# Kernel optimization log

Measured on AMD Instinct MI355X. Metric: run time of the kernel, lower is better.

The kernel has to match this reference:

```python
import jax, jax.numpy as jnp
import numpy as np

EMBED = 1024
HEADS = 16
HDIM = EMBED // HEADS
WIN = 14
RANK = 16
ALPHA = 32
MLP = 4 * EMBED


def setup_inputs() -> dict:
    key = jax.random.key(0)
    ks = jax.random.split(key, 10)
    s = 0.02
    return {
        "x": jax.random.normal(ks[0], (2, 64, 64, EMBED), jnp.float32),
        "norm1_g": jnp.ones((EMBED,), jnp.float32),
        "norm1_b": jnp.zeros((EMBED,), jnp.float32),
        "qkv_w": jax.random.normal(ks[1], (EMBED, 3 * EMBED), jnp.float32) * s,
        "qkv_b": jnp.zeros((3 * EMBED,), jnp.float32),
        "lora_a": jax.random.normal(ks[2], (EMBED, RANK), jnp.float32) * s,
        "lora_b": jax.random.normal(ks[3], (RANK, 3 * EMBED), jnp.float32) * s,
        "rel_pos_h": jax.random.normal(ks[4], (2 * WIN - 1, HDIM), jnp.float32) * s,
        "rel_pos_w": jax.random.normal(ks[5], (2 * WIN - 1, HDIM), jnp.float32) * s,
        "proj_w": jax.random.normal(ks[6], (EMBED, EMBED), jnp.float32) * s,
        "proj_b": jnp.zeros((EMBED,), jnp.float32),
        "norm2_g": jnp.ones((EMBED,), jnp.float32),
        "norm2_b": jnp.zeros((EMBED,), jnp.float32),
        "mlp_w1": jax.random.normal(ks[7], (EMBED, MLP), jnp.float32) * s,
        "mlp_b1": jnp.zeros((MLP,), jnp.float32),
        "mlp_w2": jax.random.normal(ks[8], (MLP, EMBED), jnp.float32) * s,
        "mlp_b2": jnp.zeros((EMBED,), jnp.float32),
    }


def layer_norm(x, g, b, eps=1e-6):
    mu = jnp.mean(x, axis=-1, keepdims=True)
    var = jnp.var(x, axis=-1, keepdims=True)
    return (x - mu) * jax.lax.rsqrt(var + eps) * g + b


def window_partition(x, w):
    B, H, W, C = x.shape
    ph, pw = (w - H % w) % w, (w - W % w) % w
    x = jnp.pad(x, ((0, 0), (0, ph), (0, pw), (0, 0)))
    Hp, Wp = H + ph, W + pw
    x = x.reshape(B, Hp // w, w, Wp // w, w, C)
    x = x.transpose(0, 1, 3, 2, 4, 5).reshape(-1, w, w, C)
    return x, (Hp, Wp)


def window_unpartition(x, w, pad_hw, hw):
    Hp, Wp = pad_hw
    H, W = hw
    B = x.shape[0] // (Hp // w * (Wp // w))
    x = x.reshape(B, Hp // w, Wp // w, w, w, -1)
    x = x.transpose(0, 1, 3, 2, 4, 5).reshape(B, Hp, Wp, -1)
    return x[:, :H, :W, :]


def _rel_table(rel_pos, size):
    # square windows, no interpolation: table is (2*size-1, dim)
    idx = jnp.arange(size)[:, None] - jnp.arange(size)[None, :] + (size - 1)
    return rel_pos[idx]  # (size, size, dim)


def reference(x, norm1_g, norm1_b, qkv_w, qkv_b, lora_a, lora_b,
              rel_pos_h, rel_pos_w, proj_w, proj_b, norm2_g, norm2_b,
              mlp_w1, mlp_b1, mlp_w2, mlp_b2):
    shortcut = x
    xn = layer_norm(x, norm1_g, norm1_b)
    h, w = xn.shape[1], xn.shape[2]
    xw, pad_hw = window_partition(xn, WIN)
    Bw, H, W, C = xw.shape
    N = H * W
    xf = xw.reshape(Bw, N, C)
    # QKV with LoRA injection: qkv(x) + (x @ A @ B) * alpha/rank
    qkv = xf @ qkv_w + qkv_b + (xf @ lora_a @ lora_b) * (ALPHA / RANK)
    qkv = qkv.reshape(Bw, N, 3, HEADS, HDIM).transpose(2, 0, 3, 1, 4)  # 3,Bw,h,N,d
    q, k, v = qkv[0], qkv[1], qkv[2]
    scale = HDIM ** -0.5
    attn = jnp.einsum('bhnd,bhmd->bhnm', q * scale, k)  # (Bw,heads,N,N)
    # decomposed relative position bias
    Rh = _rel_table(rel_pos_h, H)  # (H,H,d)
    Rw = _rel_table(rel_pos_w, W)  # (W,W,d)
    rq = q.reshape(Bw, HEADS, H, W, HDIM)
    rel_h = jnp.einsum('bhxyd,xkd->bhxyk', rq, Rh)  # (Bw,heads,H,W,H)
    rel_w = jnp.einsum('bhxyd,ykd->bhxyk', rq, Rw)  # (Bw,heads,H,W,W)
    attn = (attn.reshape(Bw, HEADS, H, W, H, W)
            + rel_h[..., :, None] + rel_w[..., None, :]).reshape(Bw, HEADS, N, N)
    attn = jax.nn.softmax(attn, axis=-1)
    out = jnp.einsum('bhnm,bhmd->bhnd', attn, v)
    out = out.reshape(Bw, HEADS, H, W, HDIM).transpose(0, 2, 3, 1, 4).reshape(Bw, H, W, C)
    out = out @ proj_w + proj_b
    out = window_unpartition(out, WIN, pad_hw, (h, w))
    x = shortcut + out
    # MLP with exact GELU (torch default)
    xn2 = layer_norm(x, norm2_g, norm2_b)
    hmid = jax.nn.gelu(xn2 @ mlp_w1 + mlp_b1, approximate=False)
    x = x + (hmid @ mlp_w2 + mlp_b2)
    return x
```

## Files before the change

### kernel.cpp

```cpp
#include <hip/hip_runtime.h>
#include <cstdint>
#include <cstddef>


typedef __bf16 bf16x8 __attribute__((ext_vector_type(8)));
typedef float f32x4 __attribute__((ext_vector_type(4)));

__device__ __forceinline__ unsigned short f2bf(float f) {
    unsigned u = __float_as_uint(f);
    u = (u + 0x7fffu + ((u >> 16) & 1u)) >> 16;
    return (unsigned short)u;
}
__device__ __forceinline__ float bf2f(unsigned short h) {
    return __uint_as_float(((unsigned)h) << 16);
}

#define GLDS16(gp, lp) __builtin_amdgcn_global_load_lds( \
    (__attribute__((address_space(1))) unsigned int*)(gp), \
    (__attribute__((address_space(3))) unsigned int*)(lp), 16, 0, 0)

__global__ __launch_bounds__(256) void weff_kernel(
    const float* __restrict__ W, const float* __restrict__ la,
    const float* __restrict__ lb, unsigned short* __restrict__ Wt)
{
    __shared__ float tile[32][33];
    __shared__ float lat[32][16];
    __shared__ float lbt[16][32];
    const int kb = blockIdx.x * 32, nb = blockIdx.y * 32;
    const int tn = threadIdx.x & 31, tk = threadIdx.x >> 5;
    for (int i = threadIdx.x; i < 32 * 16; i += 256)
        lat[i >> 4][i & 15] = la[(size_t)(kb + (i >> 4)) * 16 + (i & 15)];
    for (int i = threadIdx.x; i < 16 * 32; i += 256)
        lbt[i >> 5][i & 31] = lb[(size_t)(i >> 5) * 3072 + nb + (i & 31)];
#pragma unroll
    for (int i = 0; i < 4; ++i) {
        int k = tk + i * 8;
        tile[k][tn] = W[(size_t)(kb + k) * 3072 + nb + tn];
    }
    __syncthreads();
#pragma unroll
    for (int i = 0; i < 4; ++i) {
        int n = tk + i * 8;
        float acc = tile[tn][n];
#pragma unroll
        for (int r = 0; r < 16; ++r) acc += 2.0f * lat[tn][r] * lbt[r][n];
        Wt[(size_t)(nb + n) * 1024 + kb + tn] = f2bf(acc);
    }
}

__global__ __launch_bounds__(256) void transpose_bf16_kernel(
    const float* __restrict__ W, unsigned short* __restrict__ Wt,
    int Kdim, int Ndim)
{
    __shared__ float tile[32][33];
    const int kb = blockIdx.x * 32, nb = blockIdx.y * 32;
    const int tn = threadIdx.x & 31, tk = threadIdx.x >> 5;
#pragma unroll
    for (int i = 0; i < 4; ++i) {
        int k = tk + i * 8;
        tile[k][tn] = W[(size_t)(kb + k) * Ndim + nb + tn];
    }
    __syncthreads();
#pragma unroll
    for (int i = 0; i < 4; ++i) {
        int n = tk + i * 8;
        Wt[(size_t)(nb + n) * Kdim + kb + tn] = f2bf(tile[tn][n]);
    }
}

__global__ __launch_bounds__(256) void ln1_kernel(
    const float* __restrict__ x, const float* __restrict__ g,
    const float* __restrict__ b, unsigned short* __restrict__ out)
{
    const int blk = blockIdx.x;
    const int tid = threadIdx.x;
    const int bw = blk / 196, tok = blk - bw * 196;
    const int bat = bw / 25, rw = bw - bat * 25;
    const int wy = rw / 5, wx = rw - wy * 5;
    const int ty = tok / 14, tx = tok - ty * 14;
    const int y = wy * 14 + ty, xx = wx * 14 + tx;
    unsigned short* orow = out + (size_t)blk * 1024;
    if (y >= 64 || xx >= 64) {
        *(uint2*)(orow + tid * 4) = make_uint2(0u, 0u);
        return;
    }
    const float* irow = x + ((size_t)((bat * 64 + y) * 64 + xx)) * 1024;
    const float4 v = *(const float4*)(irow + tid * 4);
    float s = v.x + v.y + v.z + v.w;
    float ss = v.x * v.x + v.y * v.y + v.z * v.z + v.w * v.w;
    for (int o = 32; o > 0; o >>= 1) { s += __shfl_xor(s, o); ss += __shfl_xor(ss, o); }
    __shared__ float red[8];
    const int wave = tid >> 6, lane = tid & 63;
    if (lane == 0) { red[wave] = s; red[4 + wave] = ss; }
    __syncthreads();
    s = red[0] + red[1] + red[2] + red[3];
    ss = red[4] + red[5] + red[6] + red[7];
    const float mu = s * (1.0f / 1024.0f);
    const float var = ss * (1.0f / 1024.0f) - mu * mu;
    const float rstd = rsqrtf(var + 1e-6f);
    const float4 gv = *(const float4*)(g + tid * 4);
    const float4 bv = *(const float4*)(b + tid * 4);
    const float a0 = (v.x - mu) * rstd * gv.x + bv.x;
    const float a1 = (v.y - mu) * rstd * gv.y + bv.y;
    const float a2 = (v.z - mu) * rstd * gv.z + bv.z;
    const float a3 = (v.w - mu) * rstd * gv.w + bv.w;
    const unsigned r0 = (unsigned)f2bf(a0) | ((unsigned)f2bf(a1) << 16);
    const unsigned r1 = (unsigned)f2bf(a2) | ((unsigned)f2bf(a3) << 16);
    *(uint2*)(orow + tid * 4) = make_uint2(r0, r1);
}

__global__ __launch_bounds__(256) void ln2_kernel(
    const float* __restrict__ x, const float* __restrict__ g,
    const float* __restrict__ b, unsigned short* __restrict__ out)
{
    const int blk = blockIdx.x;
    const int tid = threadIdx.x;
    const float* irow = x + (size_t)blk * 1024;
    unsigned short* orow = out + (size_t)blk * 1024;
    const float4 v = *(const float4*)(irow + tid * 4);
    float s = v.x + v.y + v.z + v.w;
    float ss = v.x * v.x + v.y * v.y + v.z * v.z + v.w * v.w;
    for (int o = 32; o > 0; o >>= 1) { s += __shfl_xor(s, o); ss += __shfl_xor(ss, o); }
    __shared__ float red[8];
    const int wave = tid >> 6, lane = tid & 63;
    if (lane == 0) { red[wave] = s; red[4 + wave] = ss; }
    __syncthreads();
    s = red[0] + red[1] + red[2] + red[3];
    ss = red[4] + red[5] + red[6] + red[7];
    const float mu = s * (1.0f / 1024.0f);
    const float var = ss * (1.0f / 1024.0f) - mu * mu;
    const float rstd = rsqrtf(var + 1e-6f);
    const float4 gv = *(const float4*)(g + tid * 4);
    const float4 bv = *(const float4*)(b + tid * 4);
    const float a0 = (v.x - mu) * rstd * gv.x + bv.x;
    const float a1 = (v.y - mu) * rstd * gv.y + bv.y;
    const float a2 = (v.z - mu) * rstd * gv.z + bv.z;
    const float a3 = (v.w - mu) * rstd * gv.w + bv.w;
    const unsigned r0 = (unsigned)f2bf(a0) | ((unsigned)f2bf(a1) << 16);
    const unsigned r1 = (unsigned)f2bf(a2) | ((unsigned)f2bf(a3) << 16);
    *(uint2*)(orow + tid * 4) = make_uint2(r0, r1);
}

template <int EPI>
__global__ __launch_bounds__(512, 2) void gemm8p_v4(
    const unsigned short* __restrict__ A,
    const unsigned short* __restrict__ Bt,
    const float* __restrict__ bias,
    void* __restrict__ outp,
    int M, int K, int nbm, int nbn)
{
    __shared__ unsigned short As_s[2 * 16384];
    __shared__ unsigned short Bs_s[2 * 16384];

    const int tid = threadIdx.x;
    const int wave = tid >> 6, lane = tid & 63;
    const int lr = lane & 15, lq = lane >> 4;

    const int ss = (nbm + 7) >> 3;
    const int xcd = blockIdx.x & 7;
    const int sidx = blockIdx.x >> 3;
    const int ntl = sidx / ss;
    const int m_loc = sidx - ntl * ss;
    const int mt = xcd * ss + m_loc;
    if (mt >= nbm) return;
    const int m_base = mt * 256, n_base = ntl * 256;
    const int NT = K >> 6;

    const int wm = (wave >> 2) * 128;
    const int wn = (wave & 3) * 64;

    const int srow = tid >> 3, sslot = tid & 7;
    const int gch = sslot ^ (srow & 7);
    const unsigned short* a_gp[4];
    const unsigned short* b_gp[4];
#pragma unroll
    for (int u = 0; u < 4; ++u) {
        int ar = m_base + u * 64 + srow; ar = ar < M ? ar : M - 1;
        a_gp[u] = A + (size_t)ar * K + gch * 8;
        b_gp[u] = Bt + (size_t)(n_base + u * 64 + srow) * K + gch * 8;
    }
#define STG_A(t, u) GLDS16(a_gp[u] + (size_t)(t) * 64, As_s + (((t) & 1) << 14) + (u) * 4096 + tid * 8)
#define STG_B(t, u) GLDS16(b_gp[u] + (size_t)(t) * 64, Bs_s + (((t) & 1) << 14) + (u) * 4096 + tid * 8)

    const int sl0 = lq ^ (lr & 7);
    const int a_off = (wm + lr) * 64 + sl0 * 8;
    const int b_off = (wn + lr) * 64 + sl0 * 8;

    f32x4 acc[8][4] = {};

    STG_B(0, 0); STG_B(0, 1); STG_B(0, 2); STG_B(0, 3);
    STG_A(0, 0); STG_A(0, 2);
    STG_A(0, 1); STG_A(0, 3);
    asm volatile("s_waitcnt vmcnt(2)" ::: "memory");
    __builtin_amdgcn_s_barrier();

    for (int t = 0; t < NT; ++t) {
        const unsigned short* Ab = As_s + ((t & 1) << 14);
        const unsigned short* Bb = Bs_s + ((t & 1) << 14);
        bf16x8 af[4], bfv[4];
#pragma unroll
        for (int mf = 0; mf < 4; ++mf) af[mf] = *(const bf16x8*)(Ab + a_off + mf * 1024);
#pragma unroll
        for (int nf = 0; nf < 4; ++nf) bfv[nf] = *(const bf16x8*)(Bb + b_off + nf * 1024);
        if (t + 1 < NT) { STG_B(t + 1, 0); STG_B(t + 1, 1); }
        __builtin_amdgcn_s_barrier();
        asm volatile("s_waitcnt lgkmcnt(0)" ::: "memory");
        __builtin_amdgcn_sched_barrier(0);
        __builtin_amdgcn_s_setprio(1);
#pragma unroll
        for (int mf = 0; mf < 4; ++mf)
#pragma unroll
            for (int nf = 0; nf < 4; ++nf)
                acc[mf][nf] = __builtin_amdgcn_mfma_f32_16x16x32_bf16(af[mf], bfv[nf], acc[mf][nf], 0, 0, 0);
        __builtin_amdgcn_s_setprio(0);
        if (t == NT - 1) { asm volatile("s_waitcnt vmcnt(0)" ::: "memory"); }
        else             { asm volatile("s_waitcnt vmcnt(2)" ::: "memory"); }
        __builtin_amdgcn_s_barrier();
#pragma unroll
        for (int mf = 0; mf < 4; ++mf) af[mf] = *(const bf16x8*)(Ab + a_off + (4 + mf) * 1024);
        if (t + 1 < NT) { STG_B(t + 1, 2); STG_B(t + 1, 3); }
        __builtin_amdgcn_s_barrier();
        asm volatile("s_waitcnt lgkmcnt(0)" ::: "memory");
        __builtin_amdgcn_sched_barrier(0);
        __builtin_amdgcn_s_setprio(1);
#pragma unroll
        for (int mf = 0; mf < 4; ++mf)
#pragma unroll
            for (int nf = 0; nf < 4; ++nf)
                acc[4 + mf][nf] = __builtin_amdgcn_mfma_f32_16x16x32_bf16(af[mf], bfv[nf], acc[4 + mf][nf], 0, 0, 0);
        __builtin_amdgcn_s_setprio(0);
        __builtin_amdgcn_s_barrier();
#pragma unroll
        for (int mf = 0; mf < 4; ++mf) af[mf] = *(const bf16x8*)(Ab + (a_off ^ 32) + mf * 1024);
#pragma unroll
        for (int nf = 0; nf < 4; ++nf) bfv[nf] = *(const bf16x8*)(Bb + (b_off ^ 32) + nf * 1024);
        if (t + 1 < NT) { STG_A(t + 1, 0); STG_A(t + 1, 2); }
        __builtin_amdgcn_s_barrier();
        asm volatile("s_waitcnt lgkmcnt(0)" ::: "memory");
        __builtin_amdgcn_sched_barrier(0);
        __builtin_amdgcn_s_setprio(1);
#pragma unroll
        for (int mf = 0; mf < 4; ++mf)
#pragma unroll
            for (int nf = 0; nf < 4; ++nf)
                acc[mf][nf] = __builtin_amdgcn_mfma_f32_16x16x32_bf16(af[mf], bfv[nf], acc[mf][nf], 0, 0, 0);
        __builtin_amdgcn_s_setprio(0);
        __builtin_amdgcn_s_barrier();
#pragma unroll
        for (int mf = 0; mf < 4; ++mf) af[mf] = *(const bf16x8*)(Ab + (a_off ^ 32) + (4 + mf) * 1024);
        if (t + 1 < NT) { STG_A(t + 1, 1); STG_A(t + 1, 3); }
        __builtin_amdgcn_s_barrier();
        asm volatile("s_waitcnt lgkmcnt(0)" ::: "memory");
        __builtin_amdgcn_sched_barrier(0);
        __builtin_amdgcn_s_setprio(1);
#pragma unroll
        for (int mf = 0; mf < 4; ++mf)
#pragma unroll
            for (int nf = 0; nf < 4; ++nf)
                acc[4 + mf][nf] = __builtin_amdgcn_mfma_f32_16x16x32_bf16(af[mf], bfv[nf], acc[4 + mf][nf], 0, 0, 0);
        __builtin_amdgcn_s_setprio(0);
        if (t < NT - 1) { asm volatile("s_waitcnt vmcnt(2)" ::: "memory"); }
        __builtin_amdgcn_s_barrier();
    }
#undef STG_A
#undef STG_B

    float biasv[4];
#pragma unroll
    for (int j = 0; j < 4; ++j) biasv[j] = bias[n_base + wn + j * 16 + lr];

    if constexpr (EPI == 0) {
#pragma unroll
        for (int i = 0; i < 8; ++i) {
            const int m0i = m_base + wm + i * 16 + lq * 4;
            if (m0i >= M) continue;
            const int bw = m0i / 196, tok0 = m0i - bw * 196;
#pragma unroll
            for (int j = 0; j < 4; ++j) {
                const int n = n_base + wn + j * 16 + lr;
                const int which = n >> 10, hh = (n >> 6) & 15, d = n & 63;
                unsigned short* slotp = (unsigned short*)outp + (size_t)((bw * 3 + which) * 16 + hh) * 13312;
                if (which == 2) {
                    unsigned long long pv = 0;
#pragma unroll
                    for (int r = 0; r < 4; ++r)
                        pv |= (unsigned long long)f2bf(acc[i][j][r] + biasv[j]) << (16 * r);
                    *(unsigned long long*)(slotp + (size_t)d * 208 + tok0) = pv;
                } else {
#pragma unroll
                    for (int r = 0; r < 4; ++r)
                        slotp[(size_t)(tok0 + r) * 64 + d] = f2bf(acc[i][j][r] + biasv[j]);
                }
            }
        }
    } else {
#pragma unroll
        for (int i = 0; i < 8; ++i) {
#pragma unroll
            for (int r = 0; r < 4; ++r) {
                const int m = m_base + wm + i * 16 + lq * 4 + r;
                if (m >= M) continue;
#pragma unroll
                for (int j = 0; j < 4; ++j) {
                    const int n = n_base + wn + j * 16 + lr;
                    const float v = acc[i][j][r] + biasv[j];
                    const float t2 = 1.5957691216f * (v + 0.044715f * v * v * v);
                    const float e = __expf(-t2);
                    const float gl = v * __builtin_amdgcn_rcpf(1.0f + e);
                    ((unsigned short*)outp)[(size_t)m * 4096 + n] = f2bf(gl);
                }
            }
        }
    }
}

template <int EPI, int KS>
__global__ __launch_bounds__(256) void gemm_kernel(
    const unsigned short* __restrict__ A,
    const unsigned short* __restrict__ Bt,
    const float* __restrict__ bias,
    void* __restrict__ outp,
    const float* __restrict__ aux,
    int M, int K, int nbm, int nbn)
{
    __shared__ unsigned short As[2][128 * 32];
    __shared__ unsigned short Bs[2][128 * 32];
    const int tid = threadIdx.x;
    const int wave = tid >> 6, lane = tid & 63;
    const int lr = lane & 15, lq = lane >> 4;
    const int ss = (nbm + 7) >> 3;
    const int xcd = blockIdx.x & 7;
    const int s = blockIdx.x >> 3;
    const int nt2 = s / ss;
    const int m_loc = s - nt2 * ss;
    const int mt = xcd * ss + m_loc;
    if (mt >= nbm) return;
    int ks = 0, nt = nt2;
    if constexpr (KS > 1) { ks = nt2 / nbn; nt = nt2 - ks * nbn; }
    const int m_base = mt * 128, n_base = nt * 128;
    const int Kp = K / KS, kbase = ks * Kp;
    const int wm = (wave >> 1) * 64, wn = (wave & 1) * 64;
    const int N = nbn * 128;

    const int c0 = tid, c1 = tid + 256;
    const int row0 = c0 >> 2, row1 = c1 >> 2;
    const int kc = (tid & 3) ^ ((tid >> 3) & 3);
    int ar0 = m_base + row0; ar0 = ar0 < M ? ar0 : M - 1;
    int ar1 = m_base + row1; ar1 = ar1 < M ? ar1 : M - 1;
    int br0 = n_base + row0; br0 = br0 < N ? br0 : N - 1;
    int br1 = n_base + row1; br1 = br1 < N ? br1 : N - 1;
    const unsigned short* agp0 = A + (size_t)ar0 * K + kbase + kc * 8;
    const unsigned short* agp1 = A + (size_t)ar1 * K + kbase + kc * 8;
    const unsigned short* bgp0 = Bt + (size_t)br0 * K + kbase + kc * 8;
    const unsigned short* bgp1 = Bt + (size_t)br1 * K + kbase + kc * 8;
    unsigned short* alp0 = As[0] + c0 * 8;
    unsigned short* alp1 = As[0] + c1 * 8;
    unsigned short* blp0 = Bs[0] + c0 * 8;
    unsigned short* blp1 = Bs[0] + c1 * 8;
    unsigned short* alp0b = As[1] + c0 * 8;
    unsigned short* alp1b = As[1] + c1 * 8;
    unsigned short* blp0b = Bs[1] + c0 * 8;
    unsigned short* blp1b = Bs[1] + c1 * 8;

    const int swz = (lq ^ ((lr >> 1) & 3)) * 8;

    f32x4 acc[4][4] = {};

    for (int k0 = 0; k0 < Kp; k0 += 64) {
        GLDS16(agp0 + k0, alp0);
        GLDS16(agp1 + k0, alp1);
        GLDS16(bgp0 + k0, blp0);
        GLDS16(bgp1 + k0, blp1);
        GLDS16(agp0 + k0 + 32, alp0b);
        GLDS16(agp1 + k0 + 32, alp1b);
        GLDS16(bgp0 + k0 + 32, blp0b);
        GLDS16(bgp1 + k0 + 32, blp1b);
        __syncthreads();
#pragma unroll
        for (int half = 0; half < 2; ++half) {
            bf16x8 af[4], bfr[4];
#pragma unroll
            for (int i = 0; i < 4; ++i) {
                af[i]  = *(const bf16x8*)(As[half] + (wm + i * 16 + lr) * 32 + swz);
                bfr[i] = *(const bf16x8*)(Bs[half] + (wn + i * 16 + lr) * 32 + swz);
            }
#pragma unroll
            for (int i = 0; i < 4; ++i)
#pragma unroll
                for (int j = 0; j < 4; ++j)
                    acc[i][j] = __builtin_amdgcn_mfma_f32_16x16x32_bf16(af[i], bfr[j], acc[i][j], 0, 0, 0);
        }
        __syncthreads();
    }

    float biasv[4];
#pragma unroll
    for (int j = 0; j < 4; ++j)
        biasv[j] = (KS == 1 || ks == 0) ? bias[n_base + wn + j * 16 + lr] : 0.0f;

#pragma unroll
    for (int i = 0; i < 4; ++i) {
#pragma unroll
        for (int r = 0; r < 4; ++r) {
            const int m = m_base + wm + i * 16 + lq * 4 + r;
            if (m >= M) continue;
            int y = 0, xx = 0, b = 0;
            if constexpr (EPI == 1) {
                const int bw = m / 196, tok = m - bw * 196;
                b = bw / 25;
                const int rw = bw - b * 25;
                const int wy = rw / 5, wx = rw - wy * 5;
                const int ty = tok / 14, tx = tok - ty * 14;
                y = wy * 14 + ty; xx = wx * 14 + tx;
            }
#pragma unroll
            for (int j = 0; j < 4; ++j) {
                const int n = n_base + wn + j * 16 + lr;
                const float v = acc[i][j][r] + biasv[j];
                if constexpr (EPI == 1) {
                    if (y < 64 && xx < 64) {
                        const size_t idx = ((size_t)((b * 64 + y) * 64 + xx)) * 1024 + n;
                        ((float*)outp)[idx] = aux[idx] + v;
                    }
                } else {
                    const size_t idx = (size_t)m * 1024 + n;
                    if constexpr (KS > 1) atomicAdd(&((float*)outp)[idx], v);
                    else                  ((float*)outp)[idx] += v;
                }
            }
        }
    }
}

__global__ __launch_bounds__(256, 2) void attn_kernel(
    const unsigned short* __restrict__ qkv,
    const float* __restrict__ relh, const float* __restrict__ relw,
    unsigned short* __restrict__ attn_out)
{
    __shared__ unsigned short Vt[64][232];
    __shared__ unsigned short Pst[4][16][232];
    __shared__ unsigned short Db[196][28];

    const int tid = threadIdx.x;
    const int wave = tid >> 6, lane = tid & 63;
    const int lr = lane & 15, lq = lane >> 4;
    const int bw = blockIdx.x >> 4, h = blockIdx.x & 15;
    const unsigned short* qp = qkv + (size_t)((bw * 3 + 0) * 16 + h) * 13312;
    const unsigned short* kp = qkv + (size_t)((bw * 3 + 1) * 16 + h) * 13312;
    const unsigned short* vp = qkv + (size_t)((bw * 3 + 2) * 16 + h) * 13312;

    *(uint2*)&Pst[wave][lane >> 2][208 + (lane & 3) * 4] = make_uint2(0u, 0u);

    {
        unsigned short* vtf = &Vt[0][0];
        for (int idx = tid; idx < 64 * 29; idx += 256) {
            const int d = idx / 29, c = idx - d * 29;
            GLDS16(vp + d * 208 + c * 8, vtf + idx * 8);
        }
    }

    for (int t = wave; t < 28; t += 4) {
        const int isw = t >= 14;
        const int c = isw ? t - 14 : t;
        const int arow = isw ? (lr * 14 + c) : (c * 14 + lr);
        const unsigned short* ap = qp + arow * 64 + lq * 8;
        const bf16x8 a0 = *(const bf16x8*)ap;
        const bf16x8 a1 = *(const bf16x8*)(ap + 32);
        int ridx = c - lr + 13;
        ridx = ridx < 0 ? 0 : (ridx > 26 ? 26 : ridx);
        const float* tb = (isw ? relw : relh) + ridx * 64 + lq * 8;
        union BV { unsigned short u[8]; bf16x8 v; } b0, b1;
        {
            const float4 x0 = *(const float4*)tb;
            const float4 x1 = *(const float4*)(tb + 4);
            b0.u[0] = f2bf(x0.x); b0.u[1] = f2bf(x0.y); b0.u[2] = f2bf(x0.z); b0.u[3] = f2bf(x0.w);
            b0.u[4] = f2bf(x1.x); b0.u[5] = f2bf(x1.y); b0.u[6] = f2bf(x1.z); b0.u[7] = f2bf(x1.w);
            const float4 x2 = *(const float4*)(tb + 32);
            const float4 x3 = *(const float4*)(tb + 36);
            b1.u[0] = f2bf(x2.x); b1.u[1] = f2bf(x2.y); b1.u[2] = f2bf(x2.z); b1.u[3] = f2bf(x2.w);
            b1.u[4] = f2bf(x3.x); b1.u[5] = f2bf(x3.y); b1.u[6] = f2bf(x3.z); b1.u[7] = f2bf(x3.w);
        }
        f32x4 dacc = {};
        dacc = __builtin_amdgcn_mfma_f32_16x16x32_bf16(a0, b0.v, dacc, 0, 0, 0);
        dacc = __builtin_amdgcn_mfma_f32_16x16x32_bf16(a1, b1.v, dacc, 0, 0, 0);
#pragma unroll
        for (int r = 0; r < 4; ++r) {
            const int y = lq * 4 + r;
            if (y < 14 && lr < 14) {
                const int g = isw ? y * 14 + c : c * 14 + y;
                Db[g][isw ? 14 + lr : lr] = f2bf(dacc[r]);
            }
        }
    }
    __syncthreads();

    for (int mt = wave; mt < 13; mt += 4) {
        const int m0 = mt * 16;
        const unsigned short* qb = qp + (size_t)(m0 + lr) * 64 + lq * 8;
        const bf16x8 qa0 = *(const bf16x8*)qb;
        const bf16x8 qa1 = *(const bf16x8*)(qb + 32);
        f32x4 sc[13];
#pragma unroll
        for (int nt = 0; nt < 13; ++nt) {
            const unsigned short* kb = kp + (size_t)(nt * 16 + lr) * 64 + lq * 8;
            const bf16x8 k0 = *(const bf16x8*)kb;
            const bf16x8 k1 = *(const bf16x8*)(kb + 32);
            f32x4 a = {};
            a = __builtin_amdgcn_mfma_f32_16x16x32_bf16(qa0, k0, a, 0, 0, 0);
            a = __builtin_amdgcn_mfma_f32_16x16x32_bf16(qa1, k1, a, 0, 0, 0);
            sc[nt] = a;
        }
        int grow[4];
#pragma unroll
        for (int r = 0; r < 4; ++r) {
            int g = m0 + lq * 4 + r;
            grow[r] = g > 195 ? 195 : g;
        }
#pragma unroll
        for (int nt = 0; nt < 13; ++nt) {
            const int n = nt * 16 + lr;
            if (n < 196) {
                const int nx = n / 14, ny = n - nx * 14;
#pragma unroll
                for (int r = 0; r < 4; ++r)
                    sc[nt][r] = sc[nt][r] * 0.125f + bf2f(Db[grow[r]][nx]) + bf2f(Db[grow[r]][14 + ny]);
            } else {
#pragma unroll
                for (int r = 0; r < 4; ++r) sc[nt][r] = -1e30f;
            }
        }
        float rs[4];
#pragma unroll
        for (int r = 0; r < 4; ++r) {
            float mx = sc[0][r];
#pragma unroll
            for (int nt = 1; nt < 13; ++nt) mx = fmaxf(mx, sc[nt][r]);
            mx = fmaxf(mx, __shfl_xor(mx, 1));
            mx = fmaxf(mx, __shfl_xor(mx, 2));
            mx = fmaxf(mx, __shfl_xor(mx, 4));
            mx = fmaxf(mx, __shfl_xor(mx, 8));
            float s = 0.f;
#pragma unroll
            for (int nt = 0; nt < 13; ++nt) {
                const float e = __expf(sc[nt][r] - mx);
                sc[nt][r] = e;
                s += e;
            }
            s += __shfl_xor(s, 1);
            s += __shfl_xor(s, 2);
            s += __shfl_xor(s, 4);
            s += __shfl_xor(s, 8);
            rs[r] = 1.0f / s;
        }
#pragma unroll
        for (int nt = 0; nt < 13; ++nt)
#pragma unroll
            for (int r = 0; r < 4; ++r)
                Pst[wave][lq * 4 + r][nt * 16 + lr] = f2bf(sc[nt][r]);
#pragma unroll
        for (int dt = 0; dt < 4; ++dt) {
            f32x4 a = {};
#pragma unroll
            for (int ks = 0; ks < 7; ++ks) {
                const bf16x8 pa = *(const bf16x8*)&Pst[wave][lr][ks * 32 + lq * 8];
                const bf16x8 vb = *(const bf16x8*)&Vt[dt * 16 + lr][ks * 32 + lq * 8];
                a = __builtin_amdgcn_mfma_f32_16x16x32_bf16(pa, vb, a, 0, 0, 0);
            }
#pragma unroll
            for (int r = 0; r < 4; ++r) {
                const int m = m0 + lq * 4 + r;
                if (m < 196)
                    attn_out[(size_t)(bw * 196 + m) * 1024 + h * 64 + dt * 16 + lr] = f2bf(a[r] * rs[r]);
            }
        }
    }
}

extern "C" void kernel_launch(void* const* d_in, const int* in_sizes, int n_in,
                              void* d_out, int out_size, void* d_ws, size_t ws_size,
                              hipStream_t stream)
{
    (void)in_sizes; (void)n_in; (void)out_size; (void)ws_size;
    const float* x      = (const float*)d_in[0];
    const float* n1g    = (const float*)d_in[1];
    const float* n1b    = (const float*)d_in[2];
    const float* qkv_w  = (const float*)d_in[3];
    const float* qkv_b  = (const float*)d_in[4];
    const float* lora_a = (const float*)d_in[5];
    const float* lora_b = (const float*)d_in[6];
    const float* relh   = (const float*)d_in[7];
    const float* relw   = (const float*)d_in[8];
    const float* proj_w = (const float*)d_in[9];
    const float* proj_b = (const float*)d_in[10];
    const float* n2g    = (const float*)d_in[11];
    const float* n2b    = (const float*)d_in[12];
    const float* w1     = (const float*)d_in[13];
    const float* b1     = (const float*)d_in[14];
    const float* w2     = (const float*)d_in[15];
    const float* b2     = (const float*)d_in[16];
    float* out = (float*)d_out;

    char* ws = (char*)d_ws;
    size_t off = 0;
    auto alloc = [&](size_t bytes) {
        char* p = ws + off;
        off += (bytes + 255) & ~(size_t)255;
        return p;
    };
    unsigned short* weffT = (unsigned short*)alloc((size_t)3072 * 1024 * 2);
    unsigned short* projT = (unsigned short*)alloc((size_t)1024 * 1024 * 2);
    unsigned short* w1T   = (unsigned short*)alloc((size_t)4096 * 1024 * 2);
    unsigned short* w2T   = (unsigned short*)alloc((size_t)1024 * 4096 * 2);
    unsigned short* xnw   = (unsigned short*)alloc((size_t)9800 * 1024 * 2);
    unsigned short* qkvb  = (unsigned short*)alloc((size_t)8192 * 4096 * 2);
    unsigned short* attno = (unsigned short*)alloc((size_t)9800 * 1024 * 2);

    weff_kernel<<<dim3(32, 96), 256, 0, stream>>>(qkv_w, lora_a, lora_b, weffT);
    transpose_bf16_kernel<<<dim3(32, 32), 256, 0, stream>>>(proj_w, projT, 1024, 1024);
    transpose_bf16_kernel<<<dim3(32, 128), 256, 0, stream>>>(w1, w1T, 1024, 4096);
    transpose_bf16_kernel<<<dim3(128, 32), 256, 0, stream>>>(w2, w2T, 4096, 1024);
    ln1_kernel<<<9800, 256, 0, stream>>>(x, n1g, n1b, xnw);
    gemm8p_v4<0><<<dim3(8 * 5 * 12), 512, 0, stream>>>(xnw, weffT, qkv_b, qkvb, 9800, 1024, 39, 12);
    attn_kernel<<<800, 256, 0, stream>>>(qkvb, relh, relw, attno);
    gemm_kernel<1, 1><<<dim3(8 * 10 * 8), 256, 0, stream>>>(attno, projT, proj_b, out, x, 9800, 1024, 77, 8);
    unsigned short* xn2 = xnw;
    ln2_kernel<<<8192, 256, 0, stream>>>(out, n2g, n2b, xn2);
    unsigned short* hmid = qkvb;
    gemm8p_v4<2><<<dim3(8 * 4 * 16), 512, 0, stream>>>(xn2, w1T, b1, hmid, 8192, 1024, 32, 16);
    gemm_kernel<3, 2><<<dim3(8 * 8 * 16), 256, 0, stream>>>(hmid, w2T, b2, out, nullptr, 8192, 4096, 64, 8);
}
```

Measured before the change: 588.8 us.

## Merge weight transposes into one launch and drop split-K in MLP down GEMM

Three separate weight transpose launches are folded into a single kernel that picks the matrix from the block index, removing two launches. The split-K path is also removed from the generic GEMM, so the MLP down-projection now runs with full K per block and plain read-modify-write stores instead of atomic adds. This halves that GEMM's grid (512 blocks on the device), which trades atomic traffic and duplicated epilogue work for possibly lower occupancy and a longer per-block K loop.

```diff
diff --git a/kernel.cpp b/kernel.cpp
--- a/kernel.cpp
+++ b/kernel.cpp
@@ -48,12 +48,18 @@
     }
 }
 
-__global__ __launch_bounds__(256) void transpose_bf16_kernel(
-    const float* __restrict__ W, unsigned short* __restrict__ Wt,
-    int Kdim, int Ndim)
+__global__ __launch_bounds__(256) void transpose3_kernel(
+    const float* __restrict__ Wp, unsigned short* __restrict__ WpT,
+    const float* __restrict__ W1, unsigned short* __restrict__ W1T,
+    const float* __restrict__ W2, unsigned short* __restrict__ W2T)
 {
     __shared__ float tile[32][33];
-    const int kb = blockIdx.x * 32, nb = blockIdx.y * 32;
+    const int id = blockIdx.x;
+    const float* W; unsigned short* Wt; int Kdim, Ndim, kb, nb;
+    if (id < 1024)      { W = Wp; Wt = WpT; Kdim = 1024; Ndim = 1024; const int t = id;        kb = t >> 5; nb = t & 31; }
+    else if (id < 5120) { W = W1; Wt = W1T; Kdim = 1024; Ndim = 4096; const int t = id - 1024; kb = t >> 7; nb = t & 127; }
+    else                { W = W2; Wt = W2T; Kdim = 4096; Ndim = 1024; const int t = id - 5120; kb = t >> 5; nb = t & 31; }
+    kb <<= 5; nb <<= 5;
     const int tn = threadIdx.x & 31, tk = threadIdx.x >> 5;
 #pragma unroll
     for (int i = 0; i < 4; ++i) {
@@ -314,7 +320,7 @@
     }
 }
 
-template <int EPI, int KS>
+template <int EPI>
 __global__ __launch_bounds__(256) void gemm_kernel(
     const unsigned short* __restrict__ A,
     const unsigned short* __restrict__ Bt,
@@ -331,14 +337,11 @@
     const int ss = (nbm + 7) >> 3;
     const int xcd = blockIdx.x & 7;
     const int s = blockIdx.x >> 3;
-    const int nt2 = s / ss;
-    const int m_loc = s - nt2 * ss;
+    const int nt = s / ss;
+    const int m_loc = s - nt * ss;
     const int mt = xcd * ss + m_loc;
     if (mt >= nbm) return;
-    int ks = 0, nt = nt2;
-    if constexpr (KS > 1) { ks = nt2 / nbn; nt = nt2 - ks * nbn; }
     const int m_base = mt * 128, n_base = nt * 128;
-    const int Kp = K / KS, kbase = ks * Kp;
     const int wm = (wave >> 1) * 64, wn = (wave & 1) * 64;
     const int N = nbn * 128;
 
@@ -349,10 +352,10 @@
     int ar1 = m_base + row1; ar1 = ar1 < M ? ar1 : M - 1;
     int br0 = n_base + row0; br0 = br0 < N ? br0 : N - 1;
     int br1 = n_base + row1; br1 = br1 < N ? br1 : N - 1;
-    const unsigned short* agp0 = A + (size_t)ar0 * K + kbase + kc * 8;
-    const unsigned short* agp1 = A + (size_t)ar1 * K + kbase + kc * 8;
-    const unsigned short* bgp0 = Bt + (size_t)br0 * K + kbase + kc * 8;
-    const unsigned short* bgp1 = Bt + (size_t)br1 * K + kbase + kc * 8;
+    const unsigned short* agp0 = A + (size_t)ar0 * K + kc * 8;
+    const unsigned short* agp1 = A + (size_t)ar1 * K + kc * 8;
+    const unsigned short* bgp0 = Bt + (size_t)br0 * K + kc * 8;
+    const unsigned short* bgp1 = Bt + (size_t)br1 * K + kc * 8;
     unsigned short* alp0 = As[0] + c0 * 8;
     unsigned short* alp1 = As[0] + c1 * 8;
     unsigned short* blp0 = Bs[0] + c0 * 8;
@@ -366,7 +369,7 @@
 
     f32x4 acc[4][4] = {};
 
-    for (int k0 = 0; k0 < Kp; k0 += 64) {
+    for (int k0 = 0; k0 < K; k0 += 64) {
         GLDS16(agp0 + k0, alp0);
         GLDS16(agp1 + k0, alp1);
         GLDS16(bgp0 + k0, blp0);
@@ -395,8 +398,7 @@
 
     float biasv[4];
 #pragma unroll
-    for (int j = 0; j < 4; ++j)
-        biasv[j] = (KS == 1 || ks == 0) ? bias[n_base + wn + j * 16 + lr] : 0.0f;
+    for (int j = 0; j < 4; ++j) biasv[j] = bias[n_base + wn + j * 16 + lr];
 
 #pragma unroll
     for (int i = 0; i < 4; ++i) {
@@ -424,8 +426,7 @@
                     }
                 } else {
                     const size_t idx = (size_t)m * 1024 + n;
-                    if constexpr (KS > 1) atomicAdd(&((float*)outp)[idx], v);
-                    else                  ((float*)outp)[idx] += v;
+                    ((float*)outp)[idx] += v;
                 }
             }
         }
@@ -616,16 +617,14 @@
     unsigned short* attno = (unsigned short*)alloc((size_t)9800 * 1024 * 2);
 
     weff_kernel<<<dim3(32, 96), 256, 0, stream>>>(qkv_w, lora_a, lora_b, weffT);
-    transpose_bf16_kernel<<<dim3(32, 32), 256, 0, stream>>>(proj_w, projT, 1024, 1024);
-    transpose_bf16_kernel<<<dim3(32, 128), 256, 0, stream>>>(w1, w1T, 1024, 4096);
-    transpose_bf16_kernel<<<dim3(128, 32), 256, 0, stream>>>(w2, w2T, 4096, 1024);
+    transpose3_kernel<<<9216, 256, 0, stream>>>(proj_w, projT, w1, w1T, w2, w2T);
     ln1_kernel<<<9800, 256, 0, stream>>>(x, n1g, n1b, xnw);
     gemm8p_v4<0><<<dim3(8 * 5 * 12), 512, 0, stream>>>(xnw, weffT, qkv_b, qkvb, 9800, 1024, 39, 12);
     attn_kernel<<<800, 256, 0, stream>>>(qkvb, relh, relw, attno);
-    gemm_kernel<1, 1><<<dim3(8 * 10 * 8), 256, 0, stream>>>(attno, projT, proj_b, out, x, 9800, 1024, 77, 8);
+    gemm_kernel<1><<<dim3(8 * 10 * 8), 256, 0, stream>>>(attno, projT, proj_b, out, x, 9800, 1024, 77, 8);
     unsigned short* xn2 = xnw;
     ln2_kernel<<<8192, 256, 0, stream>>>(out, n2g, n2b, xn2);
     unsigned short* hmid = qkvb;
     gemm8p_v4<2><<<dim3(8 * 4 * 16), 512, 0, stream>>>(xn2, w1T, b1, hmid, 8192, 1024, 32, 16);
-    gemm_kernel<3, 2><<<dim3(8 * 8 * 16), 256, 0, stream>>>(hmid, w2T, b2, out, nullptr, 8192, 4096, 64, 8);
-}
+    gemm_kernel<3><<<dim3(8 * 8 * 8), 256, 0, stream>>>(hmid, w2T, b2, out, nullptr, 8192, 4096, 64, 8);
+}
```

After: 544.3 us, median of 2. -7.6%, faster.
